# Kernel optimization log

Measured on AMD Instinct MI355X. Metric: run time of the kernel, lower is better.

## Reference

```python
import jax, jax.numpy as jnp
import numpy as np

N = 50000      # nodes
E = 800000     # edges
F = 128        # node feature dim
H = 256        # hidden dim
A = 32         # action dim
G = 50         # graphs in batch
EPS = 1e-5     # batchnorm eps


def setup_inputs() -> dict:
    key = jax.random.key(0)
    ks = jax.random.split(key, 24)
    s = 0.02
    inp = {
        "x": jax.random.normal(ks[0], (N, F), jnp.float32),
        "edge_index": jax.random.randint(ks[1], (2, E), 0, N, jnp.int64),
        "batch": jnp.sort(jax.random.randint(ks[2], (N,), 0, G, jnp.int64)),
        "actions": jax.random.normal(ks[3], (A,), jnp.float32),
        # GCNConv weights (x @ W + b convention)
        "W1": jax.random.normal(ks[4], (F, H), jnp.float32) * s,
        "b1": jnp.zeros((H,), jnp.float32),
        "W2": jax.random.normal(ks[5], (H, H), jnp.float32) * s,
        "b2": jnp.zeros((H,), jnp.float32),
        "W3": jax.random.normal(ks[6], (H, H), jnp.float32) * s,
        "b3": jnp.zeros((H,), jnp.float32),
        # batchnorm affine params
        "g1": jnp.ones((H,), jnp.float32), "be1": jnp.zeros((H,), jnp.float32),
        "g2": jnp.ones((H,), jnp.float32), "be2": jnp.zeros((H,), jnp.float32),
        "g3": jnp.ones((H,), jnp.float32), "be3": jnp.zeros((H,), jnp.float32),
        # MLP head
        "fW1": jax.random.normal(ks[7], (H + A, H), jnp.float32) * s,
        "fb1": jnp.zeros((H,), jnp.float32),
        "fW2": jax.random.normal(ks[8], (H, H // 2), jnp.float32) * s,
        "fb2": jnp.zeros((H // 2,), jnp.float32),
        "fW3": jax.random.normal(ks[9], (H // 2, 1), jnp.float32) * s,
        "fb3": jnp.zeros((1,), jnp.float32),
    }
    return inp


def _batchnorm(h, gamma, beta):
    # training-mode batchnorm over the row dimension (biased variance, as torch)
    mu = h.mean(0)
    var = ((h - mu) ** 2).mean(0)
    return (h - mu) * jax.lax.rsqrt(var + EPS) * gamma + beta


def reference(x, edge_index, batch, actions,
              W1, b1, W2, b2, W3, b3,
              g1, be1, g2, be2, g3, be3,
              fW1, fb1, fW2, fb2, fW3, fb3):
    src, dst = edge_index[0], edge_index[1]
    n = x.shape[0]
    # GCN symmetric normalization with self-loops: deg_i = 1 + in_degree(i)
    deg = jnp.zeros((n,), x.dtype).at[dst].add(1.0) + 1.0
    dis = jax.lax.rsqrt(deg)                       # deg^{-1/2}
    enorm = dis[src] * dis[dst]                    # [E]
    self_norm = (dis * dis)[:, None]               # 1/deg_i for self-loop edge

    def gcn(h, W, b):
        h = h @ W                                  # [n,H]
        agg = jax.ops.segment_sum(h[src] * enorm[:, None], dst, num_segments=n)
        return agg + h * self_norm + b

    h = _batchnorm(jax.nn.relu(gcn(x, W1, b1)), g1, be1)   # dropout: identity (eval)
    h = _batchnorm(jax.nn.relu(gcn(h, W2, b2)), g2, be2)
    h = jax.nn.relu(gcn(h, W3, b3))

    # global_mean_pool
    counts = jax.ops.segment_sum(jnp.ones((n,), h.dtype), batch, num_segments=G)
    pooled = jax.ops.segment_sum(h, batch, num_segments=G) / jnp.maximum(counts, 1.0)[:, None]

    a = jnp.broadcast_to(actions[None, :], (G, actions.shape[0]))
    z = jnp.concatenate([pooled, a], axis=1)
    z = jax.nn.relu(z @ fW1 + fb1)
    z = _batchnorm(z, g3, be3)
    z = jax.nn.relu(z @ fW2 + fb2)
    return z @ fW3 + fb3                           # [G,1]
```

## Files before the change

### kernel.cpp

```cpp
#include <hip/hip_runtime.h>

#define NN 50000
#define NP1 (NN + 1)
#define NE 800000
#define FD 128
#define HD 256
#define AD 32
#define GN 50
#define BN_EPS 1e-5f

#define EPI_STATS 0
#define EPI_POOL  1

typedef float f32x4 __attribute__((ext_vector_type(4)));
typedef short s16x8 __attribute__((ext_vector_type(8)));

__device__ inline unsigned short f2bf(float f) {
    unsigned u = __float_as_uint(f);
    u += 0x7FFF + ((u >> 16) & 1);
    return (unsigned short)(u >> 16);
}
__device__ inline float bflo(unsigned u) { return __uint_as_float(u << 16); }
__device__ inline float bfhi(unsigned u) { return __uint_as_float(u & 0xffff0000u); }


__global__ void k_deg(const int* __restrict__ dst, int* __restrict__ counts) {
    int e = blockIdx.x * blockDim.x + threadIdx.x;
    if (e < NE) atomicAdd(&counts[dst[e]], 1);
}

__global__ void k_dis(const int* __restrict__ counts, float* __restrict__ dis) {
    int i = blockIdx.x * blockDim.x + threadIdx.x;
    if (i < NN) dis[i] = rsqrtf(1.0f + (float)counts[i]);
    if (i == 0) dis[NN] = 0.0f;
}

__global__ void k_scan1(const int* __restrict__ counts, int* __restrict__ rowptr,
                        int* __restrict__ bsum) {
    __shared__ int s[1024];
    int t = threadIdx.x;
    int i = blockIdx.x * 1024 + t;
    int v = (i < NN) ? ((counts[i] + 1) & ~1) : 0;
    s[t] = v;
    __syncthreads();
    for (int off = 1; off < 1024; off <<= 1) {
        int u = (t >= off) ? s[t - off] : 0;
        __syncthreads();
        s[t] += u;
        __syncthreads();
    }
    if (i < NN) rowptr[i + 1] = s[t];
    if (t == 1023) bsum[blockIdx.x] = s[1023];
}

__global__ void k_scan2(int* __restrict__ bsum, int* __restrict__ rowptr, int nblk) {
    if (threadIdx.x == 0 && blockIdx.x == 0) {
        int run = 0;
        for (int b = 0; b < nblk; ++b) { int t = bsum[b]; bsum[b] = run; run += t; }
        rowptr[0] = 0;
    }
}

__global__ void k_scan3(int* __restrict__ rowptr, const int* __restrict__ bsum) {
    int i = blockIdx.x * blockDim.x + threadIdx.x;
    if (i < NN) rowptr[i + 1] += bsum[i >> 10];
}

__global__ void k_csr(const int* __restrict__ src, const int* __restrict__ dst,
                      const int* __restrict__ rowptr, int* __restrict__ fill,
                      unsigned short* __restrict__ csru) {
    int e = blockIdx.x * blockDim.x + threadIdx.x;
    if (e < NE) {
        int d = dst[e];
        int p = rowptr[d] + atomicAdd(&fill[d], 1);
        csru[p] = (unsigned short)src[e];
    }
}

__global__ void k_dsum(const int* __restrict__ rowptr, const int* __restrict__ counts,
                       unsigned short* __restrict__ csru,
                       const float* __restrict__ dis, float* __restrict__ dsum) {
    int t = threadIdx.x;
    int n = blockIdx.x * 64 + (t >> 2);
    int r = t & 3;
    if (n >= NN) return;
    int e0 = rowptr[n], c = counts[n];
    if (r == 0 && (c & 1)) csru[e0 + c] = (unsigned short)NN;
    float s = 0.f;
    for (int e = e0 + r; e < e0 + c; e += 4) s += dis[csru[e]];
    s += __shfl_xor(s, 1);
    s += __shfl_xor(s, 2);
    if (r == 0) dsum[n] = s + dis[n];
}


__global__ void k_castW3(const float* __restrict__ W1, const float* __restrict__ W2,
                         const float* __restrict__ W3,
                         unsigned short* __restrict__ W1t,
                         unsigned short* __restrict__ W2t,
                         unsigned short* __restrict__ W3t) {
    int idx = blockIdx.x * 256 + threadIdx.x;
    const int N1 = FD * HD, N2 = HD * HD;
    if (idx < N1) {
        int c = idx / FD, k = idx - c * FD;
        W1t[idx] = f2bf(W1[(size_t)k * HD + c]);
    } else if (idx < N1 + N2) {
        int j = idx - N1;
        int c = j / HD, k = j - c * HD;
        W2t[j] = f2bf(W2[(size_t)k * HD + c]);
    } else if (idx < N1 + 2 * N2) {
        int j = idx - N1 - N2;
        int c = j / HD, k = j - c * HD;
        W3t[j] = f2bf(W3[(size_t)k * HD + c]);
    }
}

__global__ void k_castx(const float* __restrict__ x, const float* __restrict__ dis,
                        unsigned* __restrict__ xb, unsigned* __restrict__ tbuf) {
    int idx = blockIdx.x * 256 + threadIdx.x;
    const int total = NN * (FD / 2);
    if (idx < total) {
        int n = idx >> 6, jj = idx & 63;
        int chunk = jj >> 4, w = jj & 15;
        float sc = dis[n];
        float2 v = *(const float2*)&x[(size_t)n * FD + jj * 2];
        xb[((size_t)chunk * NP1 + n) * 16 + w] =
            ((unsigned)f2bf(v.y * sc) << 16) | f2bf(v.x * sc);
    } else {
        int q = idx - total;
        if (q < 64) xb[((size_t)(q >> 4) * NP1 + NN) * 16 + (q & 15)] = 0;
        else if (q < 192) {
            int r = q - 64;
            tbuf[((size_t)(r >> 4) * NP1 + NN) * 16 + (r & 15)] = 0;
        }
    }
}


template<int K, int EPI>
__global__ __launch_bounds__(256) void k_mm2(const unsigned* __restrict__ Ab,
                                             const unsigned short* __restrict__ Wt,
                                             const float* __restrict__ bias,
                                             const float* __restrict__ dis,
                                             unsigned short* __restrict__ Cout,
                                             float* __restrict__ stats8,
                                             const int* __restrict__ batch,
                                             const int* __restrict__ gstart,
                                             float* __restrict__ pooled) {
    __shared__ __align__(16) short Als[2][128 * 40];
    __shared__ __align__(16) short Bls[2][128 * 40];
    int t = threadIdx.x;
    int rowBase = (blockIdx.x >> 1) * 128;
    int colBase = (blockIdx.x & 1) * 128;
    int wid = t >> 6, lane = t & 63;
    int lr = lane & 15, kg = (lane >> 4) * 8;

    int task0 = t, task1 = t + 256;
    int ar0 = task0 >> 2, as0 = task0 & 3;
    int ar1 = task1 >> 2, as1 = task1 & 3;

    f32x4 acc[2][8];
#pragma unroll
    for (int i = 0; i < 2; ++i)
#pragma unroll
        for (int j = 0; j < 8; ++j) acc[i][j] = (f32x4){0.f, 0.f, 0.f, 0.f};

    {
        s16x8 v0 = (s16x8)(short)0, v1 = (s16x8)(short)0;
        if (rowBase + ar0 < NN) v0 = *(const s16x8*)&Ab[(rowBase + ar0) * 16 + as0 * 4];
        if (rowBase + ar1 < NN) v1 = *(const s16x8*)&Ab[(rowBase + ar1) * 16 + as1 * 4];
        *(s16x8*)&Als[0][ar0 * 40 + as0 * 8] = v0;
        *(s16x8*)&Als[0][ar1 * 40 + as1 * 8] = v1;
        *(s16x8*)&Bls[0][ar0 * 40 + as0 * 8] =
            *(const s16x8*)&Wt[(size_t)(colBase + ar0) * K + as0 * 8];
        *(s16x8*)&Bls[0][ar1 * 40 + as1 * 8] =
            *(const s16x8*)&Wt[(size_t)(colBase + ar1) * K + as1 * 8];
    }
    __syncthreads();

    int cur = 0;
#pragma unroll
    for (int k0 = 0; k0 < K; k0 += 32) {
        s16x8 pa0, pa1, pb0, pb1;
        bool more = (k0 + 32 < K);
        if (more) {
            const unsigned* ap = Ab + (size_t)((k0 + 32) >> 5) * NP1 * 16;
            pa0 = (s16x8)(short)0;
            pa1 = (s16x8)(short)0;
            if (rowBase + ar0 < NN) pa0 = *(const s16x8*)&ap[(rowBase + ar0) * 16 + as0 * 4];
            if (rowBase + ar1 < NN) pa1 = *(const s16x8*)&ap[(rowBase + ar1) * 16 + as1 * 4];
            pb0 = *(const s16x8*)&Wt[(size_t)(colBase + ar0) * K + k0 + 32 + as0 * 8];
            pb1 = *(const s16x8*)&Wt[(size_t)(colBase + ar1) * K + k0 + 32 + as1 * 8];
        }
        s16x8 a0 = *(const s16x8*)&Als[cur][(wid * 32 + lr) * 40 + kg];
        s16x8 a1 = *(const s16x8*)&Als[cur][(wid * 32 + 16 + lr) * 40 + kg];
#pragma unroll
        for (int nf = 0; nf < 8; ++nf) {
            s16x8 b = *(const s16x8*)&Bls[cur][(nf * 16 + lr) * 40 + kg];
            acc[0][nf] = __builtin_amdgcn_mfma_f32_16x16x32_bf16(a0, b, acc[0][nf], 0, 0, 0);
            acc[1][nf] = __builtin_amdgcn_mfma_f32_16x16x32_bf16(a1, b, acc[1][nf], 0, 0, 0);
        }
        if (more) {
            int nxt = cur ^ 1;
            *(s16x8*)&Als[nxt][ar0 * 40 + as0 * 8] = pa0;
            *(s16x8*)&Als[nxt][ar1 * 40 + as1 * 8] = pa1;
            *(s16x8*)&Bls[nxt][ar0 * 40 + as0 * 8] = pb0;
            *(s16x8*)&Bls[nxt][ar1 * 40 + as1 * 8] = pb1;
            __syncthreads();
            cur = nxt;
        }
    }

    int r4 = (lane >> 4) * 4;
    __syncthreads();
    float* ps = (float*)&Als[0][0];
    float* pq = (float*)&Bls[0][0];

    if (EPI == EPI_STATS) {
#pragma unroll
        for (int nf = 0; nf < 8; ++nf) {
            int cl = nf * 16 + lr;
            int col = colBase + cl;
            float bcol = bias[col];
            float s_ = 0.f, q_ = 0.f;
#pragma unroll
            for (int mf = 0; mf < 2; ++mf)
#pragma unroll
                for (int r = 0; r < 4; ++r) {
                    int row = rowBase + wid * 32 + mf * 16 + r4 + r;
                    bool ok = row < NN;
                    float vv = ok ? fmaxf(acc[mf][nf][r] + bcol, 0.f) : 0.f;
                    s_ += vv;
                    q_ = fmaf(vv, vv, q_);
                    if (ok)
                        Cout[((size_t)(col >> 5) * NP1 + row) * 32 + (col & 31)]
                            = f2bf(vv * dis[row]);
                }
            s_ += __shfl_xor(s_, 16); s_ += __shfl_xor(s_, 32);
            q_ += __shfl_xor(q_, 16); q_ += __shfl_xor(q_, 32);
            if (lane < 16) { ps[wid * 128 + cl] = s_; pq[wid * 128 + cl] = q_; }
        }
        __syncthreads();
        if (t < 128) {
            float ssum = ps[t] + ps[128 + t] + ps[256 + t] + ps[384 + t];
            float qsum = pq[t] + pq[128 + t] + pq[256 + t] + pq[384 + t];
            float* sb = stats8 + (size_t)((blockIdx.x >> 1) & 7) * 2 * HD;
            atomicAdd(&sb[colBase + t], ssum);
            atomicAdd(&sb[HD + colBase + t], qsum);
        }
    } else {
        int nvalid = NN - rowBase;
        int lastRow = rowBase + (nvalid < 128 ? nvalid : 128) - 1;
        int gA = batch[rowBase];
        int gB = batch[lastRow];
        if (gB - gA <= 1) {
            int split = (gB > gA) ? gstart[gB] : (rowBase + 128);
#pragma unroll
            for (int nf = 0; nf < 8; ++nf) {
                int cl = nf * 16 + lr;
                float bcol = bias[colBase + cl];
                float s_ = 0.f;
#pragma unroll
                for (int mf = 0; mf < 2; ++mf)
#pragma unroll
                    for (int r = 0; r < 4; ++r) {
                        int row = rowBase + wid * 32 + mf * 16 + r4 + r;
                        float vv = fmaxf(acc[mf][nf][r] + bcol, 0.f);
                        s_ += (row < NN && row < split) ? vv : 0.f;
                    }
                s_ += __shfl_xor(s_, 16); s_ += __shfl_xor(s_, 32);
                if (lane < 16) ps[wid * 128 + cl] = s_;
            }
            __syncthreads();
            if (t < 128) {
                float tot = ps[t] + ps[128 + t] + ps[256 + t] + ps[384 + t];
                atomicAdd(&pooled[gA * HD + colBase + t], tot);
            }
            if (gB > gA) {
                __syncthreads();
#pragma unroll
                for (int nf = 0; nf < 8; ++nf) {
                    int cl = nf * 16 + lr;
                    float bcol = bias[colBase + cl];
                    float s_ = 0.f;
#pragma unroll
                    for (int mf = 0; mf < 2; ++mf)
#pragma unroll
                        for (int r = 0; r < 4; ++r) {
                            int row = rowBase + wid * 32 + mf * 16 + r4 + r;
                            float vv = fmaxf(acc[mf][nf][r] + bcol, 0.f);
                            s_ += (row < NN && row >= split) ? vv : 0.f;
                        }
                    s_ += __shfl_xor(s_, 16); s_ += __shfl_xor(s_, 32);
                    if (lane < 16) ps[wid * 128 + cl] = s_;
                }
                __syncthreads();
                if (t < 128) {
                    float tot = ps[t] + ps[128 + t] + ps[256 + t] + ps[384 + t];
                    atomicAdd(&pooled[gB * HD + colBase + t], tot);
                }
            }
        } else {
#pragma unroll
            for (int mf = 0; mf < 2; ++mf)
#pragma unroll
                for (int r = 0; r < 4; ++r) {
                    int row = rowBase + wid * 32 + mf * 16 + r4 + r;
                    if (row < NN) {
                        int g = batch[row];
#pragma unroll
                        for (int nf = 0; nf < 8; ++nf) {
                            int col = colBase + nf * 16 + lr;
                            float vv = fmaxf(acc[mf][nf][r] + bias[col], 0.f);
                            atomicAdd(&pooled[g * HD + col], vv);
                        }
                    }
                }
        }
    }
}


template<int NCHUNK, bool AFFINE>
__global__ __launch_bounds__(256) void k_aggc(const unsigned* __restrict__ tin,
                                              const int* __restrict__ rowptr,
                                              const unsigned short* __restrict__ csru,
                                              const float* __restrict__ dis,
                                              const float* __restrict__ aff_a,
                                              const float* __restrict__ aff_c,
                                              const float* __restrict__ dsum,
                                              unsigned* __restrict__ outp) {
    int c = blockIdx.x & (NCHUNK - 1);
    int g = blockIdx.x / NCHUNK;
    int local = threadIdx.x >> 4;
    int jj = threadIdx.x & 15;
    int n = g * 16 + local;
    if (n >= NN) return;
    const unsigned* tc = tin + (size_t)c * NP1 * 16;
    unsigned u0 = tc[n * 16 + jj];
    float a0a = bflo(u0), a1a = bfhi(u0);
    float a0b = 0.f, a1b = 0.f;
    int e0 = rowptr[n], e1 = rowptr[n + 1];
    int e = e0;
    for (; e + 8 <= e1; e += 8) {
        const unsigned* p32 = (const unsigned*)(csru + e);
        unsigned i01 = p32[0], i23 = p32[1], i45 = p32[2], i67 = p32[3];
        unsigned v0 = tc[(i01 & 0xffffu) * 16 + jj];
        unsigned v1 = tc[(i01 >> 16) * 16 + jj];
        unsigned v2 = tc[(i23 & 0xffffu) * 16 + jj];
        unsigned v3 = tc[(i23 >> 16) * 16 + jj];
        unsigned v4 = tc[(i45 & 0xffffu) * 16 + jj];
        unsigned v5 = tc[(i45 >> 16) * 16 + jj];
        unsigned v6 = tc[(i67 & 0xffffu) * 16 + jj];
        unsigned v7 = tc[(i67 >> 16) * 16 + jj];
        a0a += bflo(v0); a1a += bfhi(v0);
        a0b += bflo(v1); a1b += bfhi(v1);
        a0a += bflo(v2); a1a += bfhi(v2);
        a0b += bflo(v3); a1b += bfhi(v3);
        a0a += bflo(v4); a1a += bfhi(v4);
        a0b += bflo(v5); a1b += bfhi(v5);
        a0a += bflo(v6); a1a += bfhi(v6);
        a0b += bflo(v7); a1b += bfhi(v7);
    }
    for (; e < e1; e += 2) {
        unsigned i01 = *(const unsigned*)(csru + e);
        unsigned v0 = tc[(i01 & 0xffffu) * 16 + jj];
        unsigned v1 = tc[(i01 >> 16) * 16 + jj];
        a0a += bflo(v0); a1a += bfhi(v0);
        a0b += bflo(v1); a1b += bfhi(v1);
    }
    float acc0 = a0a + a0b;
    float acc1 = a1a + a1b;
    float dn = dis[n];
    if (AFFINE) {
        float wn = dsum[n];
        int col2 = c * 16 + jj;
        float2 a2 = *(const float2*)&aff_a[2 * col2];
        float2 c2 = *(const float2*)&aff_c[2 * col2];
        acc0 = dn * fmaf(a2.x, acc0, c2.x * wn);
        acc1 = dn * fmaf(a2.y, acc1, c2.y * wn);
    } else {
        acc0 *= dn;
        acc1 *= dn;
    }
    outp[((size_t)c * NP1 + n) * 16 + jj] = ((unsigned)f2bf(acc1) << 16) | f2bf(acc0);
}


__global__ void k_affine(float* __restrict__ stats8, const float* __restrict__ g,
                         const float* __restrict__ be, float* __restrict__ a,
                         float* __restrict__ c) {
    int j = threadIdx.x;
    float s = 0.f, q = 0.f;
    for (int b = 0; b < 8; ++b) {
        s += stats8[(size_t)b * 2 * HD + j];
        q += stats8[(size_t)b * 2 * HD + HD + j];
        stats8[(size_t)b * 2 * HD + j] = 0.f;
        stats8[(size_t)b * 2 * HD + HD + j] = 0.f;
    }
    float mu = s * (1.0f / NN);
    float var = q * (1.0f / NN) - mu * mu;
    float rs = rsqrtf(var + BN_EPS);
    float aj = g[j] * rs;
    a[j] = aj;
    c[j] = be[j] - mu * aj;
}


__global__ void k_bounds(const int* __restrict__ batch, int* __restrict__ gstart) {
    int g = threadIdx.x;
    if (g <= GN) {
        int lo = 0, hi = NN;
        while (lo < hi) {
            int mid = (lo + hi) >> 1;
            if (batch[mid] < g) lo = mid + 1; else hi = mid;
        }
        gstart[g] = lo;
    }
}

__global__ void k_poolfin(float* __restrict__ pooled, const int* __restrict__ gstart) {
    int idx = blockIdx.x * blockDim.x + threadIdx.x;
    if (idx < GN * HD) {
        int g = idx >> 8;
        float c = (float)max(gstart[g + 1] - gstart[g], 1);
        pooled[idx] /= c;
    }
}


__global__ __launch_bounds__(256) void k_head1(const float* __restrict__ pooled,
                                               const float* __restrict__ actions,
                                               const float* __restrict__ fW1,
                                               const float* __restrict__ fb1,
                                               float* __restrict__ z1) {
    int g = blockIdx.x, j = threadIdx.x;
    float acc = fb1[j];
    for (int k = 0; k < HD; ++k)
        acc = fmaf(pooled[g * HD + k], fW1[k * HD + j], acc);
    for (int k = 0; k < AD; ++k)
        acc = fmaf(actions[k], fW1[(HD + k) * HD + j], acc);
    z1[g * HD + j] = fmaxf(acc, 0.f);
}

__global__ __launch_bounds__(256) void k_headbn(float* __restrict__ z1,
                                                const float* __restrict__ g3,
                                                const float* __restrict__ be3) {
    int j = threadIdx.x;
    float s = 0.f, q = 0.f;
    for (int g = 0; g < GN; ++g) {
        float v = z1[g * HD + j];
        s += v;
        q = fmaf(v, v, q);
    }
    float mu = s * (1.0f / GN);
    float var = q * (1.0f / GN) - mu * mu;
    float rs = rsqrtf(var + BN_EPS);
    float ga = g3[j], be = be3[j];
    for (int g = 0; g < GN; ++g)
        z1[g * HD + j] = fmaf((z1[g * HD + j] - mu) * rs, ga, be);
}

__global__ __launch_bounds__(128) void k_head2(const float* __restrict__ z1,
                                               const float* __restrict__ fW2,
                                               const float* __restrict__ fb2,
                                               float* __restrict__ z2) {
    int g = blockIdx.x, j = threadIdx.x;
    float acc = fb2[j];
    for (int k = 0; k < HD; ++k)
        acc = fmaf(z1[g * HD + k], fW2[k * (HD / 2) + j], acc);
    z2[g * (HD / 2) + j] = fmaxf(acc, 0.f);
}

__global__ __launch_bounds__(64) void k_head3(const float* __restrict__ z2,
                                              const float* __restrict__ fW3,
                                              const float* __restrict__ fb3,
                                              float* __restrict__ out) {
    int g = threadIdx.x;
    if (g < GN) {
        float acc = fb3[0];
        for (int k = 0; k < HD / 2; ++k)
            acc = fmaf(z2[g * (HD / 2) + k], fW3[k], acc);
        out[g] = acc;
    }
}


static inline size_t align256(size_t x) { return (x + 255) & ~(size_t)255; }

extern "C" void kernel_launch(void* const* d_in, const int* in_sizes, int n_in,
                              void* d_out, int out_size, void* d_ws, size_t ws_size,
                              hipStream_t stream) {
    const float* x       = (const float*)d_in[0];
    const int*   ei      = (const int*)d_in[1];
    const int*   batch   = (const int*)d_in[2];
    const float* actions = (const float*)d_in[3];
    const float* W1 = (const float*)d_in[4];
    const float* b1 = (const float*)d_in[5];
    const float* W2 = (const float*)d_in[6];
    const float* b2 = (const float*)d_in[7];
    const float* W3 = (const float*)d_in[8];
    const float* b3 = (const float*)d_in[9];
    const float* g1  = (const float*)d_in[10];
    const float* be1 = (const float*)d_in[11];
    const float* g2  = (const float*)d_in[12];
    const float* be2 = (const float*)d_in[13];
    const float* g3  = (const float*)d_in[14];
    const float* be3 = (const float*)d_in[15];
    const float* fW1 = (const float*)d_in[16];
    const float* fb1 = (const float*)d_in[17];
    const float* fW2 = (const float*)d_in[18];
    const float* fb2 = (const float*)d_in[19];
    const float* fW3 = (const float*)d_in[20];
    const float* fb3 = (const float*)d_in[21];
    float* out = (float*)d_out;

    const int* esrc = ei;
    const int* edst = ei + NE;

    char* p = (char*)d_ws;
    size_t off = 0;
    auto carve = [&](size_t bytes) { void* r = p + off; off = align256(off + bytes); return r; };
    unsigned* xb   = (unsigned*)carve((size_t)4 * NP1 * 16 * 4);
    unsigned* xa   = (unsigned*)carve((size_t)4 * NP1 * 16 * 4);
    unsigned* tbuf = (unsigned*)carve((size_t)8 * NP1 * 16 * 4);
    unsigned* ah   = (unsigned*)carve((size_t)8 * NP1 * 16 * 4);
    float* dis     = (float*)carve((size_t)NP1 * 4);
    int*   counts  = (int*)carve((size_t)NN * 4);
    int*   fill    = (int*)carve((size_t)NN * 4);
    int*   rowptr  = (int*)carve((size_t)(NN + 1) * 4);
    unsigned short* csru = (unsigned short*)carve((size_t)(NE + NN) * 2);
    float* dsum    = (float*)carve((size_t)NN * 4);
    int*   bsum    = (int*)carve(64 * 4);
    float* pooled  = (float*)carve((size_t)GN * HD * 4);
    int*   gstart  = (int*)carve((size_t)(GN + 1) * 4);
    float* stats8  = (float*)carve((size_t)8 * 2 * HD * 4);
    float* affa    = (float*)carve(HD * 4);
    float* affc    = (float*)carve(HD * 4);
    float* z1      = (float*)carve((size_t)GN * HD * 4);
    float* z2      = (float*)carve((size_t)GN * (HD / 2) * 4);
    unsigned short* W1t = (unsigned short*)carve((size_t)FD * HD * 2);
    unsigned short* W2t = (unsigned short*)carve((size_t)HD * HD * 2);
    unsigned short* W3t = (unsigned short*)carve((size_t)HD * HD * 2);
    (void)ws_size;

    const int TB = 256;
    const int ebk = (NE + TB - 1) / TB;
    const int nbk = (NN + TB - 1) / TB;
    const int nbk64 = (NN + 63) / 64;
    const int scanblk = (NN + 1023) / 1024;
    const int mmg2 = ((NN + 127) / 128) * 2;
    const int ngrp = NN / 16;
    const int castWblk = (FD * HD + 2 * HD * HD + 255) / 256;
    const int castxblk = (NN * (FD / 2) + 192 + 255) / 256;

    k_castW3<<<castWblk, TB, 0, stream>>>(W1, W2, W3, W1t, W2t, W3t);

    size_t cfbytes = (size_t)((char*)rowptr - (char*)counts);
    hipMemsetAsync(counts, 0, cfbytes, stream);
    k_deg<<<ebk, TB, 0, stream>>>(edst, counts);
    k_dis<<<nbk, TB, 0, stream>>>(counts, dis);
    k_scan1<<<scanblk, 1024, 0, stream>>>(counts, rowptr, bsum);
    k_scan2<<<1, 64, 0, stream>>>(bsum, rowptr, scanblk);
    k_scan3<<<nbk, TB, 0, stream>>>(rowptr, bsum);
    k_csr<<<ebk, TB, 0, stream>>>(esrc, edst, rowptr, fill, csru);
    k_dsum<<<nbk64, TB, 0, stream>>>(rowptr, counts, csru, dis, dsum);
    k_bounds<<<1, 64, 0, stream>>>(batch, gstart);

    k_castx<<<castxblk, TB, 0, stream>>>(x, dis, xb, tbuf);

    hipMemsetAsync(stats8, 0, (size_t)8 * 2 * HD * 4, stream);
    k_aggc<4, false><<<4 * ngrp, TB, 0, stream>>>(xb, rowptr, csru, dis,
                                                  nullptr, nullptr, nullptr, xa);
    k_mm2<FD, EPI_STATS><<<mmg2, TB, 0, stream>>>(xa, W1t, b1, dis, (unsigned short*)tbuf,
                                                  stats8, nullptr, nullptr, nullptr);
    k_affine<<<1, HD, 0, stream>>>(stats8, g1, be1, affa, affc);

    k_aggc<8, true><<<8 * ngrp, TB, 0, stream>>>(tbuf, rowptr, csru, dis,
                                                 affa, affc, dsum, ah);
    k_mm2<HD, EPI_STATS><<<mmg2, TB, 0, stream>>>(ah, W2t, b2, dis, (unsigned short*)tbuf,
                                                  stats8, nullptr, nullptr, nullptr);
    k_affine<<<1, HD, 0, stream>>>(stats8, g2, be2, affa, affc);

    hipMemsetAsync(pooled, 0, (size_t)GN * HD * 4, stream);
    k_aggc<8, true><<<8 * ngrp, TB, 0, stream>>>(tbuf, rowptr, csru, dis,
                                                 affa, affc, dsum, ah);
    k_mm2<HD, EPI_POOL><<<mmg2, TB, 0, stream>>>(ah, W3t, b3, dis, nullptr,
                                                 nullptr, batch, gstart, pooled);

    k_poolfin<<<(GN * HD + TB - 1) / TB, TB, 0, stream>>>(pooled, gstart);

    k_head1<<<GN, TB, 0, stream>>>(pooled, actions, fW1, fb1, z1);
    k_headbn<<<1, TB, 0, stream>>>(z1, g3, be3);
    k_head2<<<GN, 128, 0, stream>>>(z1, fW2, fb2, z2);
    k_head3<<<1, 64, 0, stream>>>(z2, fW3, fb3, out);
}
```

Measured before the change: 396.6 us.

## Aggregate each node with a full wavefront splitting edges four ways

The gather-aggregation kernel now maps one 64-lane wavefront per node instead of 16 lanes per node. The four 16-lane quarters each take every fourth edge and are combined with cross-lane shuffles. CSR rows are padded to multiples of four with a dummy zero-row index, so the edge loop has no remainder handling. This raises memory-level parallelism per node and shortens the serial edge chain. In exchange it adds padding gathers, shuffle reductions, and idle lanes during the epilogue.

```diff
diff --git a/kernel.cpp b/kernel.cpp
--- a/kernel.cpp
+++ b/kernel.cpp
@@ -40,7 +40,7 @@
     __shared__ int s[1024];
     int t = threadIdx.x;
     int i = blockIdx.x * 1024 + t;
-    int v = (i < NN) ? ((counts[i] + 1) & ~1) : 0;
+    int v = (i < NN) ? ((counts[i] + 3) & ~3) : 0;
     s[t] = v;
     __syncthreads();
     for (int off = 1; off < 1024; off <<= 1) {
@@ -85,7 +85,8 @@
     int r = t & 3;
     if (n >= NN) return;
     int e0 = rowptr[n], c = counts[n];
-    if (r == 0 && (c & 1)) csru[e0 + c] = (unsigned short)NN;
+    int cpad = (c + 3) & ~3;
+    if (c + r < cpad) csru[e0 + c + r] = (unsigned short)NN;
     float s = 0.f;
     for (int e = e0 + r; e < e0 + c; e += 4) s += dis[csru[e]];
     s += __shfl_xor(s, 1);
@@ -322,7 +323,7 @@
 
 
 template<int NCHUNK, bool AFFINE>
-__global__ __launch_bounds__(256) void k_aggc(const unsigned* __restrict__ tin,
+__global__ __launch_bounds__(256) void k_aggw(const unsigned* __restrict__ tin,
                                               const int* __restrict__ rowptr,
                                               const unsigned short* __restrict__ csru,
                                               const float* __restrict__ dis,
@@ -332,58 +333,52 @@
                                               unsigned* __restrict__ outp) {
     int c = blockIdx.x & (NCHUNK - 1);
     int g = blockIdx.x / NCHUNK;
-    int local = threadIdx.x >> 4;
-    int jj = threadIdx.x & 15;
-    int n = g * 16 + local;
+    int wv = threadIdx.x >> 6;
+    int lane = threadIdx.x & 63;
+    int q = lane >> 4, jj = lane & 15;
+    int n = g * 4 + wv;
     if (n >= NN) return;
     const unsigned* tc = tin + (size_t)c * NP1 * 16;
-    unsigned u0 = tc[n * 16 + jj];
-    float a0a = bflo(u0), a1a = bfhi(u0);
-    float a0b = 0.f, a1b = 0.f;
     int e0 = rowptr[n], e1 = rowptr[n + 1];
-    int e = e0;
-    for (; e + 8 <= e1; e += 8) {
-        const unsigned* p32 = (const unsigned*)(csru + e);
-        unsigned i01 = p32[0], i23 = p32[1], i45 = p32[2], i67 = p32[3];
-        unsigned v0 = tc[(i01 & 0xffffu) * 16 + jj];
-        unsigned v1 = tc[(i01 >> 16) * 16 + jj];
-        unsigned v2 = tc[(i23 & 0xffffu) * 16 + jj];
-        unsigned v3 = tc[(i23 >> 16) * 16 + jj];
-        unsigned v4 = tc[(i45 & 0xffffu) * 16 + jj];
-        unsigned v5 = tc[(i45 >> 16) * 16 + jj];
-        unsigned v6 = tc[(i67 & 0xffffu) * 16 + jj];
-        unsigned v7 = tc[(i67 >> 16) * 16 + jj];
-        a0a += bflo(v0); a1a += bfhi(v0);
-        a0b += bflo(v1); a1b += bfhi(v1);
-        a0a += bflo(v2); a1a += bfhi(v2);
-        a0b += bflo(v3); a1b += bfhi(v3);
-        a0a += bflo(v4); a1a += bfhi(v4);
-        a0b += bflo(v5); a1b += bfhi(v5);
-        a0a += bflo(v6); a1a += bfhi(v6);
-        a0b += bflo(v7); a1b += bfhi(v7);
-    }
-    for (; e < e1; e += 2) {
-        unsigned i01 = *(const unsigned*)(csru + e);
-        unsigned v0 = tc[(i01 & 0xffffu) * 16 + jj];
-        unsigned v1 = tc[(i01 >> 16) * 16 + jj];
-        a0a += bflo(v0); a1a += bfhi(v0);
-        a0b += bflo(v1); a1b += bfhi(v1);
-    }
-    float acc0 = a0a + a0b;
-    float acc1 = a1a + a1b;
-    float dn = dis[n];
-    if (AFFINE) {
-        float wn = dsum[n];
-        int col2 = c * 16 + jj;
-        float2 a2 = *(const float2*)&aff_a[2 * col2];
-        float2 c2 = *(const float2*)&aff_c[2 * col2];
-        acc0 = dn * fmaf(a2.x, acc0, c2.x * wn);
-        acc1 = dn * fmaf(a2.y, acc1, c2.y * wn);
-    } else {
-        acc0 *= dn;
-        acc1 *= dn;
-    }
-    outp[((size_t)c * NP1 + n) * 16 + jj] = ((unsigned)f2bf(acc1) << 16) | f2bf(acc0);
+    const unsigned short* ip = csru + e0 + q;
+    int nq = (e1 - e0) >> 2;
+    float a0 = 0.f, a1 = 0.f, b0 = 0.f, b1 = 0.f;
+    int i = 0;
+    for (; i + 2 <= nq; i += 2) {
+        unsigned idxA = ip[i * 4];
+        unsigned idxB = ip[i * 4 + 4];
+        unsigned vA = tc[idxA * 16 + jj];
+        unsigned vB = tc[idxB * 16 + jj];
+        a0 += bflo(vA); a1 += bfhi(vA);
+        b0 += bflo(vB); b1 += bfhi(vB);
+    }
+    if (i < nq) {
+        unsigned idxA = ip[i * 4];
+        unsigned vA = tc[idxA * 16 + jj];
+        a0 += bflo(vA); a1 += bfhi(vA);
+    }
+    float acc0 = a0 + b0;
+    float acc1 = a1 + b1;
+    acc0 += __shfl_xor(acc0, 16); acc0 += __shfl_xor(acc0, 32);
+    acc1 += __shfl_xor(acc1, 16); acc1 += __shfl_xor(acc1, 32);
+    if (lane < 16) {
+        unsigned u0 = tc[n * 16 + jj];
+        acc0 += bflo(u0);
+        acc1 += bfhi(u0);
+        float dn = dis[n];
+        if (AFFINE) {
+            float wn = dsum[n];
+            int col2 = c * 16 + jj;
+            float2 a2 = *(const float2*)&aff_a[2 * col2];
+            float2 c2 = *(const float2*)&aff_c[2 * col2];
+            acc0 = dn * fmaf(a2.x, acc0, c2.x * wn);
+            acc1 = dn * fmaf(a2.y, acc1, c2.y * wn);
+        } else {
+            acc0 *= dn;
+            acc1 *= dn;
+        }
+        outp[((size_t)c * NP1 + n) * 16 + jj] = ((unsigned)f2bf(acc1) << 16) | f2bf(acc0);
+    }
 }
 
 
@@ -529,7 +524,7 @@
     int*   counts  = (int*)carve((size_t)NN * 4);
     int*   fill    = (int*)carve((size_t)NN * 4);
     int*   rowptr  = (int*)carve((size_t)(NN + 1) * 4);
-    unsigned short* csru = (unsigned short*)carve((size_t)(NE + NN) * 2);
+    unsigned short* csru = (unsigned short*)carve((size_t)(NE + 3 * NN) * 2);
     float* dsum    = (float*)carve((size_t)NN * 4);
     int*   bsum    = (int*)carve(64 * 4);
     float* pooled  = (float*)carve((size_t)GN * HD * 4);
@@ -550,7 +545,7 @@
     const int nbk64 = (NN + 63) / 64;
     const int scanblk = (NN + 1023) / 1024;
     const int mmg2 = ((NN + 127) / 128) * 2;
-    const int ngrp = NN / 16;
+    const int ngrp4 = (NN + 3) / 4;
     const int castWblk = (FD * HD + 2 * HD * HD + 255) / 256;
     const int castxblk = (NN * (FD / 2) + 192 + 255) / 256;
 
@@ -570,21 +565,21 @@
     k_castx<<<castxblk, TB, 0, stream>>>(x, dis, xb, tbuf);
 
     hipMemsetAsync(stats8, 0, (size_t)8 * 2 * HD * 4, stream);
-    k_aggc<4, false><<<4 * ngrp, TB, 0, stream>>>(xb, rowptr, csru, dis,
-                                                  nullptr, nullptr, nullptr, xa);
+    k_aggw<4, false><<<4 * ngrp4, TB, 0, stream>>>(xb, rowptr, csru, dis,
+                                                   nullptr, nullptr, nullptr, xa);
     k_mm2<FD, EPI_STATS><<<mmg2, TB, 0, stream>>>(xa, W1t, b1, dis, (unsigned short*)tbuf,
                                                   stats8, nullptr, nullptr, nullptr);
     k_affine<<<1, HD, 0, stream>>>(stats8, g1, be1, affa, affc);
 
-    k_aggc<8, true><<<8 * ngrp, TB, 0, stream>>>(tbuf, rowptr, csru, dis,
-                                                 affa, affc, dsum, ah);
+    k_aggw<8, true><<<8 * ngrp4, TB, 0, stream>>>(tbuf, rowptr, csru, dis,
+                                                  affa, affc, dsum, ah);
     k_mm2<HD, EPI_STATS><<<mmg2, TB, 0, stream>>>(ah, W2t, b2, dis, (unsigned short*)tbuf,
                                                   stats8, nullptr, nullptr, nullptr);
     k_affine<<<1, HD, 0, stream>>>(stats8, g2, be2, affa, affc);
 
     hipMemsetAsync(pooled, 0, (size_t)GN * HD * 4, stream);
-    k_aggc<8, true><<<8 * ngrp, TB, 0, stream>>>(tbuf, rowptr, csru, dis,
-                                                 affa, affc, dsum, ah);
+    k_aggw<8, true><<<8 * ngrp4, TB, 0, stream>>>(tbuf, rowptr, csru, dis,
+                                                  affa, affc, dsum, ah);
     k_mm2<HD, EPI_POOL><<<mmg2, TB, 0, stream>>>(ah, W3t, b3, dis, nullptr,
                                                  nullptr, batch, gstart, pooled);
 
```

Result: slower. 555.5 us (+40.1%).
